# Performance work log

Measured on AMD Instinct MI355X. Metric: run time of the kernel, lower is better.

Reference implementation:

```python
import jax, jax.numpy as jnp
import numpy as np

IN_C = 128
OUT_C = 128
MEM = 512
HID = MEM // 2  # 256, per ParameterGenerator hidden_channels = memory_size // 2
T = 8          # number of edge types (keys of edge_feas_dict)
N = 500_000


def setup_inputs() -> dict:
    key = jax.random.key(0)
    ks = jax.random.split(key, 16)
    s = 0.02
    inp = {
        "x": jax.random.normal(ks[0], (N, IN_C), dtype=jnp.float32),
        "type_vec": jax.random.randint(ks[1], (N,), 0, T),
        "edge_feas": jax.random.normal(ks[2], (T, MEM), dtype=jnp.float32),
        # weight_generator MLP: Linear(MEM,HID) -> ReLU -> Linear(HID,HID) -> ReLU -> Linear(HID, IN_C*OUT_C)
        "wg_w1": jax.random.normal(ks[3], (MEM, HID), dtype=jnp.float32) * s,
        "wg_b1": jnp.zeros((HID,), dtype=jnp.float32),
        "wg_w2": jax.random.normal(ks[4], (HID, HID), dtype=jnp.float32) * s,
        "wg_b2": jnp.zeros((HID,), dtype=jnp.float32),
        "wg_w3": jax.random.normal(ks[5], (HID, IN_C * OUT_C), dtype=jnp.float32) * s,
        "wg_b3": jnp.zeros((IN_C * OUT_C,), dtype=jnp.float32),
        # bias_generator MLP: Linear(MEM,HID) -> ReLU -> Linear(HID,HID) -> ReLU -> Linear(HID, OUT_C)
        "bg_w1": jax.random.normal(ks[6], (MEM, HID), dtype=jnp.float32) * s,
        "bg_b1": jnp.zeros((HID,), dtype=jnp.float32),
        "bg_w2": jax.random.normal(ks[7], (HID, HID), dtype=jnp.float32) * s,
        "bg_b2": jnp.zeros((HID,), dtype=jnp.float32),
        "bg_w3": jax.random.normal(ks[8], (HID, OUT_C), dtype=jnp.float32) * s,
        "bg_b3": jnp.zeros((OUT_C,), dtype=jnp.float32),
    }
    return inp


def _mlp(m, w1, b1, w2, b2, w3, b3):
    h = jax.nn.relu(m @ w1 + b1)
    h = jax.nn.relu(h @ w2 + b2)
    return h @ w3 + b3


def reference(x, type_vec, edge_feas,
              wg_w1, wg_b1, wg_w2, wg_b2, wg_w3, wg_b3,
              bg_w1, bg_b1, bg_w2, bg_b2, bg_w3, bg_b3):
    # Generate per-type weights [T, IN_C, OUT_C] and biases [T, OUT_C]
    W = _mlp(edge_feas, wg_w1, wg_b1, wg_w2, wg_b2, wg_w3, wg_b3).reshape(T, IN_C, OUT_C)
    B = _mlp(edge_feas, bg_w1, bg_b1, bg_w2, bg_b2, bg_w3, bg_b3)  # [T, OUT_C]
    # Masked per-type linear, scattered back: out[n] = x[n] @ W[type_vec[n]] + B[type_vec[n]]
    out = jnp.zeros((x.shape[0], OUT_C), dtype=x.dtype)
    for t in range(T):  # small fixed set of types
        yt = x @ W[t] + B[t]
        out = jnp.where((type_vec == t)[:, None], yt, out)
    return out
```

## Files before the change

### kernel.cpp

```cpp
#include <hip/hip_runtime.h>
#include <hip/hip_bf16.h>

#define NT 8
#define MEMC 512
#define HID 256
#define C 128

typedef __attribute__((ext_vector_type(8))) short short8;
typedef __attribute__((ext_vector_type(4))) float f32x4;

__device__ inline short f2bf(float f) {
    union { __hip_bfloat16 b; short s; } u;
    u.b = __float2bfloat16(f);
    return u.s;
}

__global__ __launch_bounds__(256) void k1_init_genh(
    const float* __restrict__ edge_feas,
    const float* __restrict__ wg_w1, const float* __restrict__ wg_b1,
    const float* __restrict__ wg_w2, const float* __restrict__ wg_b2,
    const float* __restrict__ bg_w1, const float* __restrict__ bg_b1,
    const float* __restrict__ bg_w2, const float* __restrict__ bg_b2,
    int* __restrict__ hist, int* __restrict__ cursor,
    float* __restrict__ h_wg, float* __restrict__ h_bg)
{
    int b = blockIdx.x, tid = threadIdx.x;
    if (b == 0) {
        if (tid < NT) { hist[tid] = 0; cursor[tid * 16] = 0; }
        return;
    }
    int gb = b - 1;
    int t = gb & 7;
    int gen = gb >> 3;
    const float* w1 = gen ? bg_w1 : wg_w1;
    const float* b1 = gen ? bg_b1 : wg_b1;
    const float* w2 = gen ? bg_w2 : wg_w2;
    const float* b2 = gen ? bg_b2 : wg_b2;
    float* hout = gen ? h_bg : h_wg;

    __shared__ float m[MEMC];
    __shared__ float part[4][HID];
    __shared__ float h1[HID];
    m[tid]       = edge_feas[t * MEMC + tid];
    m[tid + 256] = edge_feas[t * MEMC + tid + 256];
    __syncthreads();

    int w = tid >> 6, l = tid & 63;
    {
        float ax = 0.f, ay = 0.f, az = 0.f, aw = 0.f;
        const float* wp = w1 + (size_t)(w * 128) * HID + 4 * l;
        #pragma unroll 8
        for (int k = 0; k < 128; ++k) {
            float4 v = *(const float4*)(wp + (size_t)k * HID);
            float mk = m[w * 128 + k];
            ax += mk * v.x; ay += mk * v.y; az += mk * v.z; aw += mk * v.w;
        }
        *(float4*)&part[w][4 * l] = make_float4(ax, ay, az, aw);
    }
    __syncthreads();
    {
        float s = part[0][tid] + part[1][tid] + part[2][tid] + part[3][tid] + b1[tid];
        h1[tid] = fmaxf(s, 0.f);
    }
    __syncthreads();
    {
        float ax = 0.f, ay = 0.f, az = 0.f, aw = 0.f;
        const float* wp = w2 + (size_t)(w * 64) * HID + 4 * l;
        #pragma unroll 8
        for (int k = 0; k < 64; ++k) {
            float4 v = *(const float4*)(wp + (size_t)k * HID);
            float hk = h1[w * 64 + k];
            ax += hk * v.x; ay += hk * v.y; az += hk * v.z; aw += hk * v.w;
        }
        *(float4*)&part[w][4 * l] = make_float4(ax, ay, az, aw);
    }
    __syncthreads();
    {
        float s = part[0][tid] + part[1][tid] + part[2][tid] + part[3][tid] + b2[tid];
        hout[t * HID + tid] = fmaxf(s, 0.f);
    }
}

__global__ __launch_bounds__(256) void k2_hist_genw(
    const int* __restrict__ type_vec, int N,
    const float* __restrict__ h_wg, const float* __restrict__ h_bg,
    const float* __restrict__ wg_w3, const float* __restrict__ wg_b3,
    const float* __restrict__ bg_w3, const float* __restrict__ bg_b3,
    int* __restrict__ hist, short* __restrict__ Wt, float* __restrict__ Bias,
    int n_hist_blocks)
{
    int b = blockIdx.x, tid = threadIdx.x;
    __shared__ float sh[2048];
    __shared__ float sp[2048];
    if (b < n_hist_blocks) {
        int lane = tid & 63, wv = tid >> 6;
        int start = b * 1024 + wv * 256;
        int cnt[NT];
        #pragma unroll
        for (int t = 0; t < NT; ++t) cnt[t] = 0;
        #pragma unroll
        for (int c = 0; c < 4; ++c) {
            int n = start + c * 64 + lane;
            int mt = (n < N) ? type_vec[n] : NT;
            #pragma unroll
            for (int t = 0; t < NT; ++t)
                cnt[t] += __popcll(__ballot(mt == t));
        }
        if (lane < NT) atomicAdd(&hist[lane], cnt[lane]);
        return;
    }
    int gb = b - n_hist_blocks;
    if (gb < 256) {
        for (int i = tid; i < 2048; i += 256) sh[i] = h_wg[i];
        __syncthreads();
        int cl = tid & 63, p = tid >> 6;
        int col = gb * 64 + cl;
        float acc[NT];
        #pragma unroll
        for (int t = 0; t < NT; ++t) acc[t] = 0.f;
        const float* wp = wg_w3 + (size_t)(p * 64) * (C * C) + col;
        #pragma unroll 8
        for (int j = 0; j < 64; ++j) {
            float v = wp[(size_t)j * (C * C)];
            #pragma unroll
            for (int t = 0; t < NT; ++t) acc[t] += sh[t * 256 + p * 64 + j] * v;
        }
        #pragma unroll
        for (int t = 0; t < NT; ++t) sp[p * 512 + t * 64 + cl] = acc[t];
        __syncthreads();
        #pragma unroll
        for (int r = 0; r < 2; ++r) {
            int o = tid + 256 * r;
            int t = o >> 6, c2 = o & 63;
            float s = sp[t * 64 + c2] + sp[512 + t * 64 + c2]
                    + sp[1024 + t * 64 + c2] + sp[1536 + t * 64 + c2]
                    + wg_b3[gb * 64 + c2];
            int flat = gb * 64 + c2;
            Wt[t * (C * C) + (flat & 127) * C + (flat >> 7)] = f2bf(s);
        }
        return;
    }
    for (int i = tid; i < 2048; i += 256) sh[i] = h_bg[i];
    __syncthreads();
    int cl = tid & 127, p = tid >> 7;
    float acc[NT];
    #pragma unroll
    for (int t = 0; t < NT; ++t) acc[t] = 0.f;
    const float* wp = bg_w3 + (size_t)(p * 128) * C + cl;
    #pragma unroll 8
    for (int j = 0; j < 128; ++j) {
        float v = wp[(size_t)j * C];
        #pragma unroll
        for (int t = 0; t < NT; ++t) acc[t] += sh[t * 256 + p * 128 + j] * v;
    }
    #pragma unroll
    for (int t = 0; t < NT; ++t) sp[p * 1024 + t * 128 + cl] = acc[t];
    __syncthreads();
    #pragma unroll
    for (int r = 0; r < 4; ++r) {
        int o = tid + 256 * r;
        int t = o >> 7, c2 = o & 127;
        Bias[t * C + c2] = sp[t * 128 + c2] + sp[1024 + t * 128 + c2] + bg_b3[c2];
    }
}

__global__ __launch_bounds__(256) void k4_scatter(
    const int* __restrict__ type_vec, int N,
    const int* __restrict__ hist, int* __restrict__ cursor,
    int* __restrict__ idx)
{
    int b = blockIdx.x, tid = threadIdx.x;
    int lane = tid & 63, wv = tid >> 6;
    __shared__ int pb[4][NT];

    int seg[NT];
    {
        int s = 0;
        #pragma unroll
        for (int t = 0; t < NT; ++t) { seg[t] = s; s += ((hist[t] + 127) >> 7) << 7; }
    }
    int start = b * 1024 + wv * 256;

    int cnt[NT];
    #pragma unroll
    for (int t = 0; t < NT; ++t) cnt[t] = 0;
    #pragma unroll
    for (int c = 0; c < 4; ++c) {
        int n = start + c * 64 + lane;
        int mt = (n < N) ? type_vec[n] : NT;
        #pragma unroll
        for (int t = 0; t < NT; ++t)
            cnt[t] += __popcll(__ballot(mt == t));
    }
    if (lane < NT) pb[wv][lane] = cnt[lane];
    __syncthreads();
    if (tid < NT) {
        int s0 = pb[0][tid], s1 = pb[1][tid], s2 = pb[2][tid], s3 = pb[3][tid];
        int base = atomicAdd(&cursor[tid * 16], s0 + s1 + s2 + s3);
        pb[0][tid] = base;
        pb[1][tid] = base + s0;
        pb[2][tid] = base + s0 + s1;
        pb[3][tid] = base + s0 + s1 + s2;
    }
    __syncthreads();
    int run[NT];
    #pragma unroll
    for (int t = 0; t < NT; ++t) run[t] = seg[t] + pb[wv][t];

    unsigned long long below = (1ULL << lane) - 1ULL;
    #pragma unroll
    for (int c = 0; c < 4; ++c) {
        int n = start + c * 64 + lane;
        int mt = (n < N) ? type_vec[n] : NT;
        int mypos = 0;
        #pragma unroll
        for (int t = 0; t < NT; ++t) {
            unsigned long long msk = __ballot(mt == t);
            if (mt == t) mypos = run[t] + __popcll(msk & below);
            run[t] += __popcll(msk);
        }
        if (n < N) idx[mypos] = n;
    }
}

__global__ __launch_bounds__(512, 4) void k5_gemm(
    const float* __restrict__ x, const int* __restrict__ idx,
    const short* __restrict__ Wt, const float* __restrict__ Bias,
    const int* __restrict__ hist, float* __restrict__ out)
{
    __shared__ short Bs[C * C];
    int tid = threadIdx.x;
    int lane = tid & 63, w = tid >> 6;
    int m16 = lane & 15, quad = lane >> 4;
    int block_base = blockIdx.x * 128;

    int seg[NT + 1], harr[NT];
    {
        int s = 0;
        #pragma unroll
        for (int t = 0; t < NT; ++t) {
            harr[t] = hist[t];
            seg[t] = s;
            s += ((harr[t] + 127) >> 7) << 7;
        }
        seg[NT] = s;
    }
    if (block_base >= seg[NT]) return;
    int t = 0;
    #pragma unroll
    for (int i = 1; i < NT; ++i)
        if (block_base >= seg[i]) t = i;
    int vlim = 0;
    #pragma unroll
    for (int i = 0; i < NT; ++i)
        if (i == t) vlim = seg[i] + harr[i];

    int row0 = block_base + 16 * w;
    int rowA = row0 + m16;
    bool validA = rowA < vlim;
    int node_a = idx[rowA];
    int na = validA ? node_a : 0;

    short8 bstg[4];
    {
        const short* wsrc = Wt + t * (C * C);
        #pragma unroll
        for (int i = 0; i < 4; ++i)
            bstg[i] = *(const short8*)(wsrc + (size_t)(i * 512 + tid) * 8);
    }

    float4 a0[4], a1[4];
    {
        const float* xr = x + (size_t)na * C + quad * 8;
        #pragma unroll
        for (int kk = 0; kk < 4; ++kk) {
            a0[kk] = *(const float4*)(xr + kk * 32);
            a1[kk] = *(const float4*)(xr + kk * 32 + 4);
        }
    }

    int node_c[4];
    bool valid_c[4];
    #pragma unroll
    for (int r = 0; r < 4; ++r) {
        int rowC = row0 + quad * 4 + r;
        valid_c[r] = rowC < vlim;
        node_c[r] = idx[rowC];
    }
    float bv[8];
    #pragma unroll
    for (int ni = 0; ni < 8; ++ni) bv[ni] = Bias[t * C + ni * 16 + m16];

    {
        #pragma unroll
        for (int i = 0; i < 4; ++i) {
            int s = i * 512 + tid;
            int row = s >> 4, sl = s & 15;
            *(short8*)((char*)Bs + row * 256 + ((sl ^ (row & 15)) << 4)) = bstg[i];
        }
    }

    __syncthreads();

    short8 af[4];
    #pragma unroll
    for (int kk = 0; kk < 4; ++kk) {
        short8 sv;
        sv[0] = f2bf(a0[kk].x); sv[1] = f2bf(a0[kk].y);
        sv[2] = f2bf(a0[kk].z); sv[3] = f2bf(a0[kk].w);
        sv[4] = f2bf(a1[kk].x); sv[5] = f2bf(a1[kk].y);
        sv[6] = f2bf(a1[kk].z); sv[7] = f2bf(a1[kk].w);
        af[kk] = sv;
    }
    if (!validA) {
        #pragma unroll
        for (int kk = 0; kk < 4; ++kk)
            af[kk] = (short8){0, 0, 0, 0, 0, 0, 0, 0};
    }

    f32x4 acc[8];
    #pragma unroll
    for (int i = 0; i < 8; ++i) acc[i] = (f32x4){0.f, 0.f, 0.f, 0.f};

    {
        const char* bbase = (const char*)Bs + m16 * 256;
        #pragma unroll
        for (int kk = 0; kk < 4; ++kk) {
            int cswz = (((kk * 4 + quad) ^ m16) << 4);
            #pragma unroll
            for (int ni = 0; ni < 8; ++ni) {
                short8 bf = *(const short8*)(bbase + (ni << 12) + cswz);
                acc[ni] = __builtin_amdgcn_mfma_f32_16x16x32_bf16(af[kk], bf, acc[ni], 0, 0, 0);
            }
        }
    }

    #pragma unroll
    for (int ni = 0; ni < 8; ++ni) {
        #pragma unroll
        for (int r = 0; r < 4; ++r) {
            if (valid_c[r])
                out[(size_t)node_c[r] * C + ni * 16 + m16] = acc[ni][r] + bv[ni];
        }
    }
}

extern "C" void kernel_launch(void* const* d_in, const int* in_sizes, int n_in,
                              void* d_out, int out_size, void* d_ws, size_t ws_size,
                              hipStream_t stream)
{
    const float* x         = (const float*)d_in[0];
    const int*   type_vec  = (const int*)d_in[1];
    const float* edge_feas = (const float*)d_in[2];
    const float* wg_w1 = (const float*)d_in[3];
    const float* wg_b1 = (const float*)d_in[4];
    const float* wg_w2 = (const float*)d_in[5];
    const float* wg_b2 = (const float*)d_in[6];
    const float* wg_w3 = (const float*)d_in[7];
    const float* wg_b3 = (const float*)d_in[8];
    const float* bg_w1 = (const float*)d_in[9];
    const float* bg_b1 = (const float*)d_in[10];
    const float* bg_w2 = (const float*)d_in[11];
    const float* bg_b2 = (const float*)d_in[12];
    const float* bg_w3 = (const float*)d_in[13];
    const float* bg_b3 = (const float*)d_in[14];
    float* out = (float*)d_out;
    int N = in_sizes[1];

    char* ws = (char*)d_ws;
    int*   hist   = (int*)(ws + 0);
    int*   cursor = (int*)(ws + 128);
    float* h_wg   = (float*)(ws + 1024);
    float* h_bg   = (float*)(ws + 9216);
    float* Bias   = (float*)(ws + 17408);
    short* Wt     = (short*)(ws + 21504);
    int*   idx    = (int*)(ws + 283648);

    int nblk128 = (N + 127) / 128;
    int n_hist  = (N + 1023) / 1024;

    k1_init_genh<<<17, 256, 0, stream>>>(
        edge_feas, wg_w1, wg_b1, wg_w2, wg_b2, bg_w1, bg_b1, bg_w2, bg_b2,
        hist, cursor, h_wg, h_bg);

    k2_hist_genw<<<n_hist + 257, 256, 0, stream>>>(
        type_vec, N, h_wg, h_bg, wg_w3, wg_b3, bg_w3, bg_b3,
        hist, Wt, Bias, n_hist);

    k4_scatter<<<n_hist, 256, 0, stream>>>(
        type_vec, N, hist, cursor, idx);

    k5_gemm<<<nblk128 + 8, 512, 0, stream>>>(x, idx, Wt, Bias, hist, out);
}
```

Before: 538.2 us.

## Make grouped GEMM persistent with per-block tile chunks and A-prefetch

The per-type GEMM changes from one 128-row tile per 512-thread block to a fixed grid of 2048 blocks of 256 threads. Each block walks a contiguous chunk of 64-row tiles, and segment padding drops from 128 to 64 rows. The weight tile in LDS is reloaded only when the type changes, and the next tile's gathered x rows are prefetched while MFMAs run on the current one. This targets the repeated per-block staging of the 32KB weight tile and exposed gather latency, at the cost of fewer concurrent waves per tile and more register pressure from the prefetch buffers.

```diff
diff --git a/kernel.cpp b/kernel.cpp
--- a/kernel.cpp
+++ b/kernel.cpp
@@ -177,7 +177,7 @@
     {
         int s = 0;
         #pragma unroll
-        for (int t = 0; t < NT; ++t) { seg[t] = s; s += ((hist[t] + 127) >> 7) << 7; }
+        for (int t = 0; t < NT; ++t) { seg[t] = s; s += ((hist[t] + 63) >> 6) << 6; }
     }
     int start = b * 1024 + wv * 256;
 
@@ -223,16 +223,16 @@
     }
 }
 
-__global__ __launch_bounds__(512, 4) void k5_gemm(
+__global__ __launch_bounds__(256, 4) void k5_gemm(
     const float* __restrict__ x, const int* __restrict__ idx,
     const short* __restrict__ Wt, const float* __restrict__ Bias,
-    const int* __restrict__ hist, float* __restrict__ out)
+    const int* __restrict__ hist, float* __restrict__ out,
+    int chunk)
 {
     __shared__ short Bs[C * C];
     int tid = threadIdx.x;
     int lane = tid & 63, w = tid >> 6;
     int m16 = lane & 15, quad = lane >> 4;
-    int block_base = blockIdx.x * 128;
 
     int seg[NT + 1], harr[NT];
     {
@@ -241,107 +241,133 @@
         for (int t = 0; t < NT; ++t) {
             harr[t] = hist[t];
             seg[t] = s;
-            s += ((harr[t] + 127) >> 7) << 7;
+            s += ((harr[t] + 63) >> 6) << 6;
         }
         seg[NT] = s;
     }
-    if (block_base >= seg[NT]) return;
-    int t = 0;
-    #pragma unroll
-    for (int i = 1; i < NT; ++i)
-        if (block_base >= seg[i]) t = i;
-    int vlim = 0;
-    #pragma unroll
-    for (int i = 0; i < NT; ++i)
-        if (i == t) vlim = seg[i] + harr[i];
-
-    int row0 = block_base + 16 * w;
-    int rowA = row0 + m16;
-    bool validA = rowA < vlim;
-    int node_a = idx[rowA];
-    int na = validA ? node_a : 0;
-
-    short8 bstg[4];
-    {
+    int ntiles = seg[NT] >> 6;
+    int tile0 = blockIdx.x * chunk;
+    int tile1 = tile0 + chunk; if (tile1 > ntiles) tile1 = ntiles;
+    if (tile0 >= tile1) return;
+
+    float bv[8];
+    float4 pa0[4], pa1[4];
+    int pnodeC[4];
+
+    auto typeOf = [&](int tile) {
+        int bb = tile << 6, t = 0;
+        #pragma unroll
+        for (int i = 1; i < NT; ++i) if (bb >= seg[i]) t = i;
+        return t;
+    };
+    auto vlimOf = [&](int t) {
+        int v = 0;
+        #pragma unroll
+        for (int i = 0; i < NT; ++i) if (i == t) v = seg[i] + harr[i];
+        return v;
+    };
+    auto stageB = [&](int t) {
         const short* wsrc = Wt + t * (C * C);
-        #pragma unroll
-        for (int i = 0; i < 4; ++i)
-            bstg[i] = *(const short8*)(wsrc + (size_t)(i * 512 + tid) * 8);
-    }
-
-    float4 a0[4], a1[4];
-    {
-        const float* xr = x + (size_t)na * C + quad * 8;
-        #pragma unroll
-        for (int kk = 0; kk < 4; ++kk) {
-            a0[kk] = *(const float4*)(xr + kk * 32);
-            a1[kk] = *(const float4*)(xr + kk * 32 + 4);
-        }
-    }
-
-    int node_c[4];
-    bool valid_c[4];
-    #pragma unroll
-    for (int r = 0; r < 4; ++r) {
-        int rowC = row0 + quad * 4 + r;
-        valid_c[r] = rowC < vlim;
-        node_c[r] = idx[rowC];
-    }
-    float bv[8];
-    #pragma unroll
-    for (int ni = 0; ni < 8; ++ni) bv[ni] = Bias[t * C + ni * 16 + m16];
-
-    {
-        #pragma unroll
-        for (int i = 0; i < 4; ++i) {
-            int s = i * 512 + tid;
+        short8 bstg[8];
+        #pragma unroll
+        for (int i = 0; i < 8; ++i)
+            bstg[i] = *(const short8*)(wsrc + (size_t)(i * 256 + tid) * 8);
+        #pragma unroll
+        for (int i = 0; i < 8; ++i) {
+            int s = i * 256 + tid;
             int row = s >> 4, sl = s & 15;
             *(short8*)((char*)Bs + row * 256 + ((sl ^ (row & 15)) << 4)) = bstg[i];
         }
-    }
-
-    __syncthreads();
-
-    short8 af[4];
-    #pragma unroll
-    for (int kk = 0; kk < 4; ++kk) {
-        short8 sv;
-        sv[0] = f2bf(a0[kk].x); sv[1] = f2bf(a0[kk].y);
-        sv[2] = f2bf(a0[kk].z); sv[3] = f2bf(a0[kk].w);
-        sv[4] = f2bf(a1[kk].x); sv[5] = f2bf(a1[kk].y);
-        sv[6] = f2bf(a1[kk].z); sv[7] = f2bf(a1[kk].w);
-        af[kk] = sv;
-    }
-    if (!validA) {
-        #pragma unroll
-        for (int kk = 0; kk < 4; ++kk)
-            af[kk] = (short8){0, 0, 0, 0, 0, 0, 0, 0};
-    }
-
-    f32x4 acc[8];
-    #pragma unroll
-    for (int i = 0; i < 8; ++i) acc[i] = (f32x4){0.f, 0.f, 0.f, 0.f};
-
-    {
-        const char* bbase = (const char*)Bs + m16 * 256;
+        #pragma unroll
+        for (int ni = 0; ni < 8; ++ni) bv[ni] = Bias[t * C + ni * 16 + m16];
+    };
+    auto prefA = [&](int tile, int vlim) {
+        int rA = (tile << 6) + 16 * w + m16;
+        int na = (rA < vlim) ? idx[rA] : 0;
+        const float* xr = x + (size_t)na * C + quad * 8;
         #pragma unroll
         for (int kk = 0; kk < 4; ++kk) {
-            int cswz = (((kk * 4 + quad) ^ m16) << 4);
+            pa0[kk] = *(const float4*)(xr + kk * 32);
+            pa1[kk] = *(const float4*)(xr + kk * 32 + 4);
+        }
+    };
+    auto prefC = [&](int tile) {
+        int r0 = (tile << 6) + 16 * w + quad * 4;
+        #pragma unroll
+        for (int r = 0; r < 4; ++r) pnodeC[r] = idx[r0 + r];
+    };
+
+    int cur_t = typeOf(tile0);
+    int cur_vlim = vlimOf(cur_t);
+    stageB(cur_t);
+    prefA(tile0, cur_vlim);
+    prefC(tile0);
+    __syncthreads();
+
+    int tile = tile0;
+    while (true) {
+        short8 af[4];
+        #pragma unroll
+        for (int kk = 0; kk < 4; ++kk) {
+            short8 sv;
+            sv[0] = f2bf(pa0[kk].x); sv[1] = f2bf(pa0[kk].y);
+            sv[2] = f2bf(pa0[kk].z); sv[3] = f2bf(pa0[kk].w);
+            sv[4] = f2bf(pa1[kk].x); sv[5] = f2bf(pa1[kk].y);
+            sv[6] = f2bf(pa1[kk].z); sv[7] = f2bf(pa1[kk].w);
+            af[kk] = sv;
+        }
+        if (((tile << 6) + 16 * w + m16) >= cur_vlim) {
+            #pragma unroll
+            for (int kk = 0; kk < 4; ++kk)
+                af[kk] = (short8){0, 0, 0, 0, 0, 0, 0, 0};
+        }
+
+        int next = tile + 1;
+        bool have = next < tile1;
+        int nt_ = have ? typeOf(next) : cur_t;
+        bool same = have && (nt_ == cur_t);
+        if (same) prefA(next, cur_vlim);
+
+        f32x4 acc[8];
+        #pragma unroll
+        for (int i = 0; i < 8; ++i) acc[i] = (f32x4){0.f, 0.f, 0.f, 0.f};
+        {
+            const char* bbase = (const char*)Bs + m16 * 256;
+            #pragma unroll
+            for (int kk = 0; kk < 4; ++kk) {
+                int cswz = (((kk * 4 + quad) ^ m16) << 4);
+                #pragma unroll
+                for (int ni = 0; ni < 8; ++ni) {
+                    short8 bf = *(const short8*)(bbase + (ni << 12) + cswz);
+                    acc[ni] = __builtin_amdgcn_mfma_f32_16x16x32_bf16(af[kk], bf, acc[ni], 0, 0, 0);
+                }
+            }
+        }
+
+        {
+            int rbase = (tile << 6) + 16 * w + quad * 4;
             #pragma unroll
             for (int ni = 0; ni < 8; ++ni) {
-                short8 bf = *(const short8*)(bbase + (ni << 12) + cswz);
-                acc[ni] = __builtin_amdgcn_mfma_f32_16x16x32_bf16(af[kk], bf, acc[ni], 0, 0, 0);
+                #pragma unroll
+                for (int r = 0; r < 4; ++r) {
+                    if (rbase + r < cur_vlim)
+                        out[(size_t)pnodeC[r] * C + ni * 16 + m16] = acc[ni][r] + bv[ni];
+                }
             }
         }
-    }
-
-    #pragma unroll
-    for (int ni = 0; ni < 8; ++ni) {
-        #pragma unroll
-        for (int r = 0; r < 4; ++r) {
-            if (valid_c[r])
-                out[(size_t)node_c[r] * C + ni * 16 + m16] = acc[ni][r] + bv[ni];
-        }
+
+        if (!have) break;
+        if (same) {
+            prefC(next);
+        } else {
+            __syncthreads();
+            stageB(nt_);
+            cur_t = nt_; cur_vlim = vlimOf(nt_);
+            __syncthreads();
+            prefA(next, cur_vlim);
+            prefC(next);
+        }
+        tile = next;
     }
 }
 
@@ -376,8 +402,11 @@
     short* Wt     = (short*)(ws + 21504);
     int*   idx    = (int*)(ws + 283648);
 
-    int nblk128 = (N + 127) / 128;
+    int nblk64  = (N + 63) / 64;
     int n_hist  = (N + 1023) / 1024;
+    int max_tiles = nblk64 + 8;
+    int G = 2048;
+    int chunk = (max_tiles + G - 1) / G;
 
     k1_init_genh<<<17, 256, 0, stream>>>(
         edge_feas, wg_w1, wg_b1, wg_w2, wg_b2, bg_w1, bg_b1, bg_w2, bg_b2,
@@ -390,5 +419,5 @@
     k4_scatter<<<n_hist, 256, 0, stream>>>(
         type_vec, N, hist, cursor, idx);
 
-    k5_gemm<<<nblk128 + 8, 512, 0, stream>>>(x, idx, Wt, Bias, hist, out);
-}
+    k5_gemm<<<G, 256, 0, stream>>>(x, idx, Wt, Bias, hist, out, chunk);
+}
```

Result: no change. 538.4 us (+0.0%).
